# Optimization experiments

Hardware: AMD Instinct MI355X
Metric: run time of the kernel (lower is better)

The kernel has to match this reference:

```python
import jax, jax.numpy as jnp
import numpy as np

WINDOW = 512
STEP = WINDOW // 2            # 256
NC = WINDOW // 2 + 1          # 257 rfft coeffs
N_SAMPLES = 32768
N_FRAMES = N_SAMPLES // STEP  # 128
N_ITEMS = 4096


def setup_inputs() -> dict:
    key = jax.random.key(0)
    k1, k2, k3 = jax.random.split(key, 3)
    selections = jax.random.normal(k1, (8, 32, 4, N_ITEMS), dtype=jnp.float32)
    # init: uniform(-6, 6) * bernoulli(p=0.01)  -> sparse mag/phase logits
    vals = jax.random.uniform(k2, (N_ITEMS, 2 * NC), minval=-6.0, maxval=6.0, dtype=jnp.float32)
    mask = (jax.random.uniform(k3, (N_ITEMS, 2 * NC)) < 0.01).astype(jnp.float32)
    items = vals * mask
    return {"selections": selections, "items": items}


def _resonance(mags, phases):
    # mags: (..., NC) in (0,1); phases: (..., NC) in (-pi, pi)
    k = jnp.arange(1, N_FRAMES + 1, dtype=mags.dtype)              # frame exponents
    # frame-wise decay: mag ** frame_index, computed as exp(k*log(mag))
    frame_mags = jnp.exp(jnp.log(mags)[..., None, :] * k[:, None])  # (..., F, NC)
    ph = phases[..., None, :]
    spec = jax.lax.complex(frame_mags * jnp.cos(ph), frame_mags * jnp.sin(ph))  # (..., F, NC)
    frames = jnp.fft.irfft(spec, n=WINDOW, axis=-1)                 # (..., F, WINDOW)
    # Hann window (COLA at hop = WINDOW/2)
    win = (0.5 - 0.5 * jnp.cos(2.0 * np.pi * jnp.arange(WINDOW) / WINDOW)).astype(frames.dtype)
    frames = frames * win
    lead = frames.shape[:-2]
    first = frames[..., :STEP].reshape(*lead, N_FRAMES * STEP)
    second = frames[..., STEP:].reshape(*lead, N_FRAMES * STEP)
    # overlap-add with hop STEP, truncated to N_SAMPLES
    out = first.at[..., STEP:].add(second[..., :-STEP])
    return out  # (..., N_SAMPLES)


def reference(selections, items):
    # softmax item selection over the codebook
    w = jax.nn.softmax(selections, axis=-1)                  # (B,E,X,I)
    selected = jnp.einsum('bexi,ic->bexc', w, items)         # (B,E,X,2*NC)
    mags = jax.nn.sigmoid(selected[..., :NC]) * 0.9999
    phases = jnp.tanh(selected[..., NC:]) * np.pi
    res = _resonance(mags, phases)                           # (B,E,X,N_SAMPLES)
    return res.reshape(*selected.shape[:3], -1)
```

## Files before the change

kernel.cpp:

```cpp
#include <hip/hip_runtime.h>

#define PI_F 3.14159265358979f
#define CAP 256

#if __has_builtin(__builtin_amdgcn_exp2f)
#define EXP2F(x) __builtin_amdgcn_exp2f(x)
#else
#define EXP2F(x) exp2f(x)
#endif

typedef float cf2 __attribute__((ext_vector_type(2)));
__device__ __forceinline__ cf2 mkc(float x, float y){ cf2 r; r.x = x; r.y = y; return r; }
__device__ __forceinline__ cf2 cmulv(cf2 a, cf2 b){
    cf2 bs = mkc(-b.y, b.x);
#if __has_builtin(__builtin_elementwise_fma)
    return __builtin_elementwise_fma(a.yy, bs, a.xx * b);
#else
    return a.xx * b + a.yy * bs;
#endif
}
__device__ __forceinline__ cf2 cjg(cf2 a){ return mkc(a.x, -a.y); }
__device__ __forceinline__ cf2 ci(cf2 a){ return mkc(-a.y, a.x); }

__device__ __forceinline__ void cfence() {
    asm volatile("" ::: "memory");
}

#define W16_C8 0.923879532511287f
#define W16_S8 0.382683432365090f
#define W16_R2 0.707106781186548f
__device__ __forceinline__ void idft16_full(cf2* x)
{
    cf2 u[16];
#pragma unroll
    for (int b0 = 0; b0 < 4; ++b0) {
        cf2 x0 = x[b0], x1 = x[4+b0], x2 = x[8+b0], x3 = x[12+b0];
        cf2 t0 = x0 + x2, t1 = x0 - x2;
        cf2 t2 = x1 + x3, t3 = x1 - x3;
        cf2 it3 = ci(t3);
        u[b0*4+0] = t0 + t2;
        u[b0*4+1] = t1 + it3;
        u[b0*4+2] = t0 - t2;
        u[b0*4+3] = t1 - it3;
    }
    u[4+1]  = cmulv(u[4+1],  mkc( W16_C8,  W16_S8));
    u[4+2]  = cmulv(u[4+2],  mkc( W16_R2,  W16_R2));
    u[4+3]  = cmulv(u[4+3],  mkc( W16_S8,  W16_C8));
    u[8+1]  = cmulv(u[8+1],  mkc( W16_R2,  W16_R2));
    u[8+2]  = ci(u[8+2]);
    u[8+3]  = cmulv(u[8+3],  mkc(-W16_R2,  W16_R2));
    u[12+1] = cmulv(u[12+1], mkc( W16_S8,  W16_C8));
    u[12+2] = cmulv(u[12+2], mkc(-W16_R2,  W16_R2));
    u[12+3] = cmulv(u[12+3], mkc(-W16_C8, -W16_S8));
#pragma unroll
    for (int a0 = 0; a0 < 4; ++a0) {
        cf2 x0 = u[a0], x1 = u[4+a0], x2 = u[8+a0], x3 = u[12+a0];
        cf2 t0 = x0 + x2, t1 = x0 - x2;
        cf2 t2 = x1 + x3, t3 = x1 - x3;
        cf2 it3 = ci(t3);
        x[a0+0]  = t0 + t2;
        x[a0+4]  = t1 + it3;
        x[a0+8]  = t0 - t2;
        x[a0+12] = t1 - it3;
    }
}
__device__ __forceinline__ void idft16_low8(cf2* x)
{
    cf2 u[16];
#pragma unroll
    for (int b0 = 0; b0 < 4; ++b0) {
        cf2 x0 = x[b0], x1 = x[4+b0], x2 = x[8+b0], x3 = x[12+b0];
        cf2 t0 = x0 + x2, t1 = x0 - x2;
        cf2 t2 = x1 + x3, t3 = x1 - x3;
        cf2 it3 = ci(t3);
        u[b0*4+0] = t0 + t2;
        u[b0*4+1] = t1 + it3;
        u[b0*4+2] = t0 - t2;
        u[b0*4+3] = t1 - it3;
    }
    u[4+1]  = cmulv(u[4+1],  mkc( W16_C8,  W16_S8));
    u[4+2]  = cmulv(u[4+2],  mkc( W16_R2,  W16_R2));
    u[4+3]  = cmulv(u[4+3],  mkc( W16_S8,  W16_C8));
    u[8+1]  = cmulv(u[8+1],  mkc( W16_R2,  W16_R2));
    u[8+2]  = ci(u[8+2]);
    u[8+3]  = cmulv(u[8+3],  mkc(-W16_R2,  W16_R2));
    u[12+1] = cmulv(u[12+1], mkc( W16_S8,  W16_C8));
    u[12+2] = cmulv(u[12+2], mkc(-W16_R2,  W16_R2));
    u[12+3] = cmulv(u[12+3], mkc(-W16_C8, -W16_S8));
#pragma unroll
    for (int a0 = 0; a0 < 4; ++a0) {
        cf2 x0 = u[a0], x1 = u[4+a0], x2 = u[8+a0], x3 = u[12+a0];
        cf2 t0 = x0 + x2, t1 = x0 - x2;
        cf2 t2 = x1 + x3, t3 = x1 - x3;
        cf2 it3 = ci(t3);
        x[a0+0] = t0 + t2;
        x[a0+4] = t1 + it3;
    }
}

__global__ __launch_bounds__(256) void ksoft(const float* __restrict__ sel,
                                             float* __restrict__ rowmax,
                                             float* __restrict__ rowinv)
{
    const int row = blockIdx.x;
    const int tid = threadIdx.x;
    const float4* p4 = (const float4*)(sel + (size_t)row * 4096);
    float4 v[4];
    float mx = -3.0e38f;
#pragma unroll
    for (int i = 0; i < 4; ++i) {
        v[i] = p4[tid + (i<<8)];
        mx = fmaxf(mx, fmaxf(fmaxf(v[i].x, v[i].y), fmaxf(v[i].z, v[i].w)));
    }
#pragma unroll
    for (int o = 32; o >= 1; o >>= 1) mx = fmaxf(mx, __shfl_xor(mx, o));
    __shared__ float red[8];
    const int wv = tid >> 6;
    if ((tid & 63) == 0) red[wv] = mx;
    __syncthreads();
    mx = fmaxf(fmaxf(red[0], red[1]), fmaxf(red[2], red[3]));
    float s = 0.0f;
#pragma unroll
    for (int i = 0; i < 4; ++i) {
        s += __expf(v[i].x - mx) + __expf(v[i].y - mx) + __expf(v[i].z - mx) + __expf(v[i].w - mx);
    }
#pragma unroll
    for (int o = 32; o >= 1; o >>= 1) s += __shfl_xor(s, o);
    if ((tid & 63) == 0) red[4 + wv] = s;
    __syncthreads();
    if (tid == 0) {
        rowmax[row] = mx;
        rowinv[row] = 1.0f / (red[4] + red[5] + red[6] + red[7]);
    }
}

__global__ __launch_bounds__(256) void kT(const float* __restrict__ sel,
                                          const float* __restrict__ rowmax,
                                          const float* __restrict__ rowinv,
                                          float* __restrict__ WT)
{
    __shared__ float tile[64][65];
    __shared__ float smx[64], sinv[64];
    const int t = threadIdx.x;
    const int k0 = blockIdx.x * 64;
    const int m0 = blockIdx.y * 64;

    if (t < 64) { smx[t] = rowmax[m0 + t]; sinv[t] = rowinv[m0 + t]; }
    __syncthreads();

    const int m_l = t >> 4;
    const int k_l4 = (t & 15) << 2;
#pragma unroll
    for (int i = 0; i < 4; ++i) {
        const int ml = m_l + (i << 4);
        const float mxv = smx[ml], invv = sinv[ml];
        float4 v = *(const float4*)(sel + (size_t)(m0 + ml) * 4096 + k0 + k_l4);
        tile[k_l4 + 0][ml] = __expf(v.x - mxv) * invv;
        tile[k_l4 + 1][ml] = __expf(v.y - mxv) * invv;
        tile[k_l4 + 2][ml] = __expf(v.z - mxv) * invv;
        tile[k_l4 + 3][ml] = __expf(v.w - mxv) * invv;
    }
    __syncthreads();

    const int k_l = t >> 2;
    const int mb = (t & 3) << 2;
#pragma unroll
    for (int i = 0; i < 4; ++i) {
        const int ml = mb + (i << 4);
        float4 w = make_float4(tile[k_l][ml], tile[k_l][ml+1], tile[k_l][ml+2], tile[k_l][ml+3]);
        *(float4*)(WT + (size_t)(k0 + k_l) * 1024 + m0 + ml) = w;
    }
}

__global__ __launch_bounds__(256) void kfill(const float* __restrict__ items,
                                             int* __restrict__ kidx,
                                             float* __restrict__ kval,
                                             int* __restrict__ ncol)
{
    const int c = blockIdx.x;
    const int t = threadIdx.x;
    const int wv = t >> 6;
    const int lane = t & 63;
    __shared__ int wcnt[4];

    const int kc0 = wv << 10;
    float vv[16];
    int cnt = 0;
#pragma unroll
    for (int it = 0; it < 16; ++it) {
        const int k = kc0 + (it << 6) + lane;
        const float v = items[(size_t)k * 514 + c];
        vv[it] = v;
        unsigned long long mb = __ballot(v != 0.0f);
        cnt += __popcll(mb);
    }
    if (lane == 0) wcnt[wv] = cnt;
    __syncthreads();

    int base = 0;
#pragma unroll
    for (int q = 0; q < 4; ++q) if (q < wv) base += wcnt[q];

    const unsigned long long ltmask = (lane == 63) ? 0x7fffffffffffffffull
                                                   : ((1ull << lane) - 1ull);
#pragma unroll
    for (int it = 0; it < 16; ++it) {
        const float v = vv[it];
        const bool nz = (v != 0.0f);
        unsigned long long mb = __ballot(nz);
        if (nz) {
            const int slot = base + __popcll(mb & ltmask);
            if (slot < CAP) {
                kidx[c * CAP + slot] = kc0 + (it << 6) + lane;
                kval[c * CAP + slot] = v;
            }
        }
        base += __popcll(mb);
    }
    if (t == 0) ncol[c] = wcnt[0] + wcnt[1] + wcnt[2] + wcnt[3];
}

__global__ __launch_bounds__(256) void kspmm(const float* __restrict__ WT,
                                             const int* __restrict__ kidx,
                                             const float* __restrict__ kval,
                                             const int* __restrict__ ncol,
                                             float2* __restrict__ P2)
{
    __shared__ int   ski[CAP];
    __shared__ float skv[CAP];
    const int c = blockIdx.y;
    const int m = (blockIdx.x << 8) + threadIdx.x;
    const int nn = min(ncol[c], CAP);
    if (threadIdx.x < nn) {
        ski[threadIdx.x] = kidx[c * CAP + threadIdx.x];
        skv[threadIdx.x] = kval[c * CAP + threadIdx.x];
    }
    __syncthreads();

    float acc = 0.0f;
    int i = 0;
    for (; i + 4 <= nn; i += 4) {
        const int k0 = ski[i], k1 = ski[i+1], k2 = ski[i+2], k3 = ski[i+3];
        const float v0 = skv[i], v1 = skv[i+1], v2 = skv[i+2], v3 = skv[i+3];
        const float w0 = WT[(size_t)k0 * 1024 + m];
        const float w1 = WT[(size_t)k1 * 1024 + m];
        const float w2 = WT[(size_t)k2 * 1024 + m];
        const float w3 = WT[(size_t)k3 * 1024 + m];
        acc = fmaf(v0, w0, acc);
        acc = fmaf(v1, w1, acc);
        acc = fmaf(v2, w2, acc);
        acc = fmaf(v3, w3, acc);
    }
    for (; i < nn; ++i) {
        acc = fmaf(skv[i], WT[(size_t)ski[i] * 1024 + m], acc);
    }

    const float x = acc;
    if (c < 257) {
        float mm = 0.9999f / (1.0f + __expf(-x));
        P2[((size_t)m * 257 + c) * 2] = make_float2(__log2f(mm), mm);
    } else {
        float e2 = __expf(2.0f * x);
        float th = (e2 - 1.0f) / (e2 + 1.0f);
        float ph = PI_F * th;
        float sn, cs;
        __sincosf(ph, &sn, &cs);
        P2[((size_t)m * 257 + (c - 257)) * 2 + 1] = make_float2(cs, sn);
    }
}

__global__ __launch_bounds__(256) void kres(const float4* __restrict__ P4, float* __restrict__ out)
{
    const int tid = threadIdx.x;
    const int lane = tid & 63;
    const int wv = tid >> 6;
    const int g = lane >> 4;
    const int gl = lane & 15;
    const int item = blockIdx.x >> 3;
    const int jg = blockIdx.x & 7;

    __shared__ cf2 U[16 * 256];
    cf2* ub = U + (wv * 4 + g) * 256;

    const int j = jg * 16 + wv * 4 + g;
    const float fj = (float)j;
    const float gf = (j > 0) ? 1.0f : 0.0f;
    const float sg = (gl & 1) ? -gf : gf;

    const int pb4 = item * 257;

    cf2 S[16];
#pragma unroll
    for (int r = 0; r < 16; ++r) {
        float4 q = P4[pb4 + gl + 16*r];
        float p = EXP2F(fj * q.x);
        cf2 F = p * mkc(q.z, q.w);
        cf2 Sv = (q.y + sg) * F;
        cf2 Vv = (q.y - sg) * F;
        if (gl == 0 && r == 0) { Sv.y = 0.0f; Vv.y = 0.0f; }
        S[r] = Sv;
        ub[gl + 16*r] = Vv;
    }
    float4 q6 = P4[pb4 + 256];
    float pc6 = EXP2F(fj * q6.x) * q6.z;
    const float S6 = (q6.y + gf) * pc6;
    const float V6 = (q6.y - gf) * pc6;
    cfence();

    float H6;
#pragma unroll
    for (int r = 0; r < 16; ++r) {
        const int c = gl + 16*r;
        const int im = (c == 0) ? 1 : c - 1;
        cf2 Vm = ub[im];
        if (c == 0) Vm.y = -Vm.y;
        cf2 Vp;
        if (r == 15) Vp = (gl == 15) ? mkc(V6, 0.0f) : ub[c + 1];
        else         Vp = ub[c + 1];
        S[r] = 0.5f * S[r] - 0.25f * (Vm + Vp);
    }
    H6 = 0.5f*S6 - 0.5f*ub[255].x;
    cfence();

#pragma unroll
    for (int r = 0; r < 16; ++r) ub[gl + 16*r] = S[r];
    cfence();

    cf2 zw0;
    {
        float s, c;
        __sincosf((6.283185307179586f/512.0f) * (float)gl, &s, &c);
        zw0 = mkc(c, s);
    }
    const float ZKC[16] = { 1.0f, 0.980785280403230f, 0.923879532511287f, 0.831469612302545f,
                            0.707106781186548f, 0.555570233019602f, 0.382683432365090f, 0.195090322016128f,
                            0.0f, -0.195090322016128f, -0.382683432365090f, -0.555570233019602f,
                            -0.707106781186548f, -0.831469612302545f, -0.923879532511287f, -0.980785280403230f };
    const float ZKS[16] = { 0.0f, 0.195090322016128f, 0.382683432365090f, 0.555570233019602f,
                            0.707106781186548f, 0.831469612302545f, 0.923879532511287f, 0.980785280403230f,
                            1.0f, 0.980785280403230f, 0.923879532511287f, 0.831469612302545f,
                            0.707106781186548f, 0.555570233019602f, 0.382683432365090f, 0.195090322016128f };
#pragma unroll
    for (int r = 0; r < 16; ++r) {
        const int c = gl + 16*r;
        cf2 Hk = S[r];
        cf2 cHm;
        if (r == 0) cHm = (gl == 0) ? mkc(H6, 0.0f) : cjg(ub[256 - c]);
        else        cHm = cjg(ub[256 - c]);
        cf2 w = cmulv(mkc(ZKC[r], ZKS[r]), zw0);
        cf2 A = Hk + cHm;
        cf2 B = Hk - cHm;
        S[r] = (A + cmulv(ci(w), B)) * (1.0f/512.0f);
    }
    cfence();

    idft16_full(S);

    {
        cf2 wt = cmulv(zw0, zw0);
        cf2 ww = mkc(1.0f, 0.0f);
#pragma unroll
        for (int n1 = 0; n1 < 16; ++n1) {
            ub[(gl << 4) | (n1 ^ gl)] = cmulv(S[n1], ww);
            ww = cmulv(ww, wt);
        }
    }
    cfence();

    cf2 T[16];
#pragma unroll
    for (int k1 = 0; k1 < 16; ++k1) T[k1] = ub[(k1 << 4) | (gl ^ k1)];

    idft16_low8(T);

    cf2* o2 = (cf2*)out + (size_t)item * 16384 + (j << 7);
#pragma unroll
    for (int n2 = 0; n2 < 8; ++n2) o2[gl + 16*n2] = T[n2];
}

extern "C" void kernel_launch(void* const* d_in, const int* in_sizes, int n_in,
                              void* d_out, int out_size, void* d_ws, size_t ws_size,
                              hipStream_t stream)
{
    const float* sel   = (const float*)d_in[0];
    const float* items = (const float*)d_in[1];
    float* out = (float*)d_out;
    float* ws  = (float*)d_ws;

    float* WT     = out;
    float* rowmax = out + 4194304;
    float* rowinv = out + 4195328;
    int*   ncol   = (int*)(out + 4196352);
    int*   kidx   = (int*)(out + 4196866);
    float* kval   = (float*)(out + 4196866 + 514*CAP);
    float4* P4    = (float4*)ws;

    ksoft<<<1024, 256, 0, stream>>>(sel, rowmax, rowinv);
    kT<<<dim3(64, 16), 256, 0, stream>>>(sel, rowmax, rowinv, WT);
    kfill<<<514, 256, 0, stream>>>(items, kidx, kval, ncol);
    kspmm<<<dim3(4, 514), 256, 0, stream>>>(WT, kidx, kval, ncol, (float2*)ws);
    kres<<<8192, 256, 0, stream>>>(P4, out);
}
```

Measured before the change: 103.6 us.

## Fuse softmax stats with sparse column fill; use hardware sin/cos twiddles

Merges the row softmax-statistics kernel and the sparse column-index fill kernel into one launch, with block index selecting the role, which removes a kernel launch and lets both independent jobs run concurrently. In the resonance kernel, the 1/512 normalization is folded into the exp2 exponent as a -9 offset, and the twiddle factors are computed directly with v_sin/v_cos revolution instructions instead of a recurrence of complex multiplies. This trades some accuracy assumptions on the hardware trig for fewer dependent multiplies and fewer launches.

Result: slower. 106.0 us (+2.4%).

```diff
diff --git a/kernel.cpp b/kernel.cpp
--- a/kernel.cpp
+++ b/kernel.cpp
@@ -8,6 +8,9 @@
 #else
 #define EXP2F(x) exp2f(x)
 #endif
+
+__device__ __forceinline__ float hw_sin_rev(float q){ float r; asm("v_sin_f32 %0, %1" : "=v"(r) : "v"(q)); return r; }
+__device__ __forceinline__ float hw_cos_rev(float q){ float r; asm("v_cos_f32 %0, %1" : "=v"(r) : "v"(q)); return r; }
 
 typedef float cf2 __attribute__((ext_vector_type(2)));
 __device__ __forceinline__ cf2 mkc(float x, float y){ cf2 r; r.x = x; r.y = y; return r; }
@@ -98,39 +101,87 @@
     }
 }
 
-__global__ __launch_bounds__(256) void ksoft(const float* __restrict__ sel,
-                                             float* __restrict__ rowmax,
-                                             float* __restrict__ rowinv)
-{
-    const int row = blockIdx.x;
+__global__ __launch_bounds__(256) void kfused(const float* __restrict__ sel,
+                                              const float* __restrict__ items,
+                                              float* __restrict__ rowmax,
+                                              float* __restrict__ rowinv,
+                                              int* __restrict__ kidx,
+                                              float* __restrict__ kval,
+                                              int* __restrict__ ncol)
+{
     const int tid = threadIdx.x;
-    const float4* p4 = (const float4*)(sel + (size_t)row * 4096);
-    float4 v[4];
-    float mx = -3.0e38f;
-#pragma unroll
-    for (int i = 0; i < 4; ++i) {
-        v[i] = p4[tid + (i<<8)];
-        mx = fmaxf(mx, fmaxf(fmaxf(v[i].x, v[i].y), fmaxf(v[i].z, v[i].w)));
-    }
-#pragma unroll
-    for (int o = 32; o >= 1; o >>= 1) mx = fmaxf(mx, __shfl_xor(mx, o));
-    __shared__ float red[8];
-    const int wv = tid >> 6;
-    if ((tid & 63) == 0) red[wv] = mx;
-    __syncthreads();
-    mx = fmaxf(fmaxf(red[0], red[1]), fmaxf(red[2], red[3]));
-    float s = 0.0f;
-#pragma unroll
-    for (int i = 0; i < 4; ++i) {
-        s += __expf(v[i].x - mx) + __expf(v[i].y - mx) + __expf(v[i].z - mx) + __expf(v[i].w - mx);
-    }
-#pragma unroll
-    for (int o = 32; o >= 1; o >>= 1) s += __shfl_xor(s, o);
-    if ((tid & 63) == 0) red[4 + wv] = s;
-    __syncthreads();
-    if (tid == 0) {
-        rowmax[row] = mx;
-        rowinv[row] = 1.0f / (red[4] + red[5] + red[6] + red[7]);
+    if (blockIdx.x < 1024) {
+        const int row = blockIdx.x;
+        const float4* p4 = (const float4*)(sel + (size_t)row * 4096);
+        float4 v[4];
+        float mx = -3.0e38f;
+#pragma unroll
+        for (int i = 0; i < 4; ++i) {
+            v[i] = p4[tid + (i<<8)];
+            mx = fmaxf(mx, fmaxf(fmaxf(v[i].x, v[i].y), fmaxf(v[i].z, v[i].w)));
+        }
+#pragma unroll
+        for (int o = 32; o >= 1; o >>= 1) mx = fmaxf(mx, __shfl_xor(mx, o));
+        __shared__ float red[8];
+        const int wv = tid >> 6;
+        if ((tid & 63) == 0) red[wv] = mx;
+        __syncthreads();
+        mx = fmaxf(fmaxf(red[0], red[1]), fmaxf(red[2], red[3]));
+        float s = 0.0f;
+#pragma unroll
+        for (int i = 0; i < 4; ++i) {
+            s += __expf(v[i].x - mx) + __expf(v[i].y - mx) + __expf(v[i].z - mx) + __expf(v[i].w - mx);
+        }
+#pragma unroll
+        for (int o = 32; o >= 1; o >>= 1) s += __shfl_xor(s, o);
+        if ((tid & 63) == 0) red[4 + wv] = s;
+        __syncthreads();
+        if (tid == 0) {
+            rowmax[row] = mx;
+            rowinv[row] = 1.0f / (red[4] + red[5] + red[6] + red[7]);
+        }
+    } else {
+        const int c = blockIdx.x - 1024;
+        if (c >= 514) return;
+        const int wv = tid >> 6;
+        const int lane = tid & 63;
+        __shared__ int wcnt[4];
+
+        const int kc0 = wv << 10;
+        float vv[16];
+        int cnt = 0;
+#pragma unroll
+        for (int it = 0; it < 16; ++it) {
+            const int k = kc0 + (it << 6) + lane;
+            const float v = items[(size_t)k * 514 + c];
+            vv[it] = v;
+            unsigned long long mb = __ballot(v != 0.0f);
+            cnt += __popcll(mb);
+        }
+        if (lane == 0) wcnt[wv] = cnt;
+        __syncthreads();
+
+        int base = 0;
+#pragma unroll
+        for (int q = 0; q < 4; ++q) if (q < wv) base += wcnt[q];
+
+        const unsigned long long ltmask = (lane == 63) ? 0x7fffffffffffffffull
+                                                       : ((1ull << lane) - 1ull);
+#pragma unroll
+        for (int it = 0; it < 16; ++it) {
+            const float v = vv[it];
+            const bool nz = (v != 0.0f);
+            unsigned long long mb = __ballot(nz);
+            if (nz) {
+                const int slot = base + __popcll(mb & ltmask);
+                if (slot < CAP) {
+                    kidx[c * CAP + slot] = kc0 + (it << 6) + lane;
+                    kval[c * CAP + slot] = v;
+                }
+            }
+            base += __popcll(mb);
+        }
+        if (tid == 0) ncol[c] = wcnt[0] + wcnt[1] + wcnt[2] + wcnt[3];
     }
 }
 
@@ -170,54 +221,6 @@
         float4 w = make_float4(tile[k_l][ml], tile[k_l][ml+1], tile[k_l][ml+2], tile[k_l][ml+3]);
         *(float4*)(WT + (size_t)(k0 + k_l) * 1024 + m0 + ml) = w;
     }
-}
-
-__global__ __launch_bounds__(256) void kfill(const float* __restrict__ items,
-                                             int* __restrict__ kidx,
-                                             float* __restrict__ kval,
-                                             int* __restrict__ ncol)
-{
-    const int c = blockIdx.x;
-    const int t = threadIdx.x;
-    const int wv = t >> 6;
-    const int lane = t & 63;
-    __shared__ int wcnt[4];
-
-    const int kc0 = wv << 10;
-    float vv[16];
-    int cnt = 0;
-#pragma unroll
-    for (int it = 0; it < 16; ++it) {
-        const int k = kc0 + (it << 6) + lane;
-        const float v = items[(size_t)k * 514 + c];
-        vv[it] = v;
-        unsigned long long mb = __ballot(v != 0.0f);
-        cnt += __popcll(mb);
-    }
-    if (lane == 0) wcnt[wv] = cnt;
-    __syncthreads();
-
-    int base = 0;
-#pragma unroll
-    for (int q = 0; q < 4; ++q) if (q < wv) base += wcnt[q];
-
-    const unsigned long long ltmask = (lane == 63) ? 0x7fffffffffffffffull
-                                                   : ((1ull << lane) - 1ull);
-#pragma unroll
-    for (int it = 0; it < 16; ++it) {
-        const float v = vv[it];
-        const bool nz = (v != 0.0f);
-        unsigned long long mb = __ballot(nz);
-        if (nz) {
-            const int slot = base + __popcll(mb & ltmask);
-            if (slot < CAP) {
-                kidx[c * CAP + slot] = kc0 + (it << 6) + lane;
-                kval[c * CAP + slot] = v;
-            }
-        }
-        base += __popcll(mb);
-    }
-    if (t == 0) ncol[c] = wcnt[0] + wcnt[1] + wcnt[2] + wcnt[3];
 }
 
 __global__ __launch_bounds__(256) void kspmm(const float* __restrict__ WT,
@@ -293,7 +296,7 @@
 #pragma unroll
     for (int r = 0; r < 16; ++r) {
         float4 q = P4[pb4 + gl + 16*r];
-        float p = EXP2F(fj * q.x);
+        float p = EXP2F(fmaf(fj, q.x, -9.0f));
         cf2 F = p * mkc(q.z, q.w);
         cf2 Sv = (q.y + sg) * F;
         cf2 Vv = (q.y - sg) * F;
@@ -302,7 +305,7 @@
         ub[gl + 16*r] = Vv;
     }
     float4 q6 = P4[pb4 + 256];
-    float pc6 = EXP2F(fj * q6.x) * q6.z;
+    float pc6 = EXP2F(fmaf(fj, q6.x, -9.0f)) * q6.z;
     const float S6 = (q6.y + gf) * pc6;
     const float V6 = (q6.y - gf) * pc6;
     cfence();
@@ -326,12 +329,8 @@
     for (int r = 0; r < 16; ++r) ub[gl + 16*r] = S[r];
     cfence();
 
-    cf2 zw0;
-    {
-        float s, c;
-        __sincosf((6.283185307179586f/512.0f) * (float)gl, &s, &c);
-        zw0 = mkc(c, s);
-    }
+    cf2 zw0 = mkc(hw_cos_rev((float)gl * (1.0f/512.0f)),
+                  hw_sin_rev((float)gl * (1.0f/512.0f)));
     const float ZKC[16] = { 1.0f, 0.980785280403230f, 0.923879532511287f, 0.831469612302545f,
                             0.707106781186548f, 0.555570233019602f, 0.382683432365090f, 0.195090322016128f,
                             0.0f, -0.195090322016128f, -0.382683432365090f, -0.555570233019602f,
@@ -350,19 +349,20 @@
         cf2 w = cmulv(mkc(ZKC[r], ZKS[r]), zw0);
         cf2 A = Hk + cHm;
         cf2 B = Hk - cHm;
-        S[r] = (A + cmulv(ci(w), B)) * (1.0f/512.0f);
+        S[r] = A + cmulv(ci(w), B);
     }
     cfence();
 
     idft16_full(S);
 
     {
-        cf2 wt = cmulv(zw0, zw0);
-        cf2 ww = mkc(1.0f, 0.0f);
-#pragma unroll
-        for (int n1 = 0; n1 < 16; ++n1) {
+        const float glf = (float)gl * (1.0f/256.0f);
+        ub[(gl << 4) | (0 ^ gl)] = S[0];
+#pragma unroll
+        for (int n1 = 1; n1 < 16; ++n1) {
+            const float q = (float)n1 * glf;
+            cf2 ww = mkc(hw_cos_rev(q), hw_sin_rev(q));
             ub[(gl << 4) | (n1 ^ gl)] = cmulv(S[n1], ww);
-            ww = cmulv(ww, wt);
         }
     }
     cfence();
@@ -395,9 +395,8 @@
     float* kval   = (float*)(out + 4196866 + 514*CAP);
     float4* P4    = (float4*)ws;
 
-    ksoft<<<1024, 256, 0, stream>>>(sel, rowmax, rowinv);
+    kfused<<<1538, 256, 0, stream>>>(sel, items, rowmax, rowinv, kidx, kval, ncol);
     kT<<<dim3(64, 16), 256, 0, stream>>>(sel, rowmax, rowinv, WT);
-    kfill<<<514, 256, 0, stream>>>(items, kidx, kval, ncol);
     kspmm<<<dim3(4, 514), 256, 0, stream>>>(WT, kidx, kval, ncol, (float2*)ws);
     kres<<<8192, 256, 0, stream>>>(P4, out);
 }
```
